# Optimization experiments

Hardware: AMD Instinct MI355X
Metric: run time of the kernel (lower is better)

The kernel has to match this reference:

```python
import jax, jax.numpy as jnp
import numpy as np

B, O, D = 4096, 256, 256  # batch, size_out (rules), size_in (features)


def setup_inputs() -> dict:
    key = jax.random.key(0)
    k1, k2, k3, k4, k5 = jax.random.split(key, 5)
    return {
        "x": jax.random.normal(k1, (B, D), dtype=jnp.float32),
        "scales": jax.random.normal(k2, (O, D), dtype=jnp.float32),
        # strict upper triangle holds the packed rot vectors (original inits them to zeros;
        # small values keep the quadratic form well conditioned)
        "rots": jax.random.normal(k3, (O, D, D), dtype=jnp.float32) * 0.02,
        "centroids": jax.random.normal(k4, (O, D, 1), dtype=jnp.float32),
        "b": jax.random.uniform(k5, (O,), dtype=jnp.float32, minval=0.5, maxval=1.5),
    }


def reference(x, scales, rots, centroids, b):
    # Build symmetric transform A[o] = diag(scales[o]) + triu(rots[o],1) + triu(rots[o],1)^T
    # (equivalent to the loop of diag_embed(r_i, i+1) + mirrored lower diagonal).
    upper = jnp.triu(rots, 1)                                   # [O,D,D]
    A = upper + jnp.swapaxes(upper, -1, -2)
    A = A + jnp.eye(D, dtype=scales.dtype) * scales[:, None, :]  # diag_embed(scales)
    # Augmented affine map: mul[o,i,b'] = A[o] @ x[b'] + centroid[o,i]; const row dropped
    # since only the first size_in rows feed the norm.
    y = jnp.einsum('bj,oij->boi', x, A) + centroids[..., 0][None, :, :]  # [B,O,D]
    rx = jnp.sqrt(jnp.sum(y * y, axis=-1))                      # L2 norm over D -> [B,O]
    return 1.0 / (1.0 + rx ** (2.0 * b))                        # bell membership [B,O]
```

## Files before the change

kernel.cpp:

```cpp
#include <hip/hip_runtime.h>
#include <cstdint>
#include <cmath>

#define Bn 4096
#define Dn 256
#define On 256

typedef __bf16 v8bf __attribute__((ext_vector_type(8)));
typedef float  v4f  __attribute__((ext_vector_type(4)));
typedef unsigned short us8 __attribute__((ext_vector_type(8)));

__device__ __forceinline__ unsigned short f2bf(float f) {
    unsigned int u = __builtin_bit_cast(unsigned int, f);
    unsigned int r = (u + 0x7fffu + ((u >> 16) & 1u)) >> 16;
    return (unsigned short)r;
}

__device__ __forceinline__ void gl_lds16(const void* g, void* l) {
    __builtin_amdgcn_global_load_lds(
        (const __attribute__((address_space(1))) void*)(uintptr_t)g,
        (__attribute__((address_space(3))) void*)(uintptr_t)l, 16, 0, 0);
}

__global__ __launch_bounds__(256) void prep(
    const float* __restrict__ scales, const float* __restrict__ rots,
    const float* __restrict__ x, unsigned short* __restrict__ Ap,
    unsigned short* __restrict__ xb) {
    const int bid = blockIdx.x;
    const int tid = threadIdx.x;

    if (bid >= 2560) {
        const int cb = bid - 2560;
#pragma unroll
        for (int s = 0; s < 4; ++s) {
            const int i = cb * 4096 + s * 1024 + tid * 4;
            const float4 v = *(const float4*)(x + i);
            ushort4 u;
            u.x = f2bf(v.x); u.y = f2bf(v.y); u.z = f2bf(v.z); u.w = f2bf(v.w);
            *(ushort4*)(xb + i) = u;
        }
        return;
    }

    static const int TI[10] = {0, 0, 0, 0, 1, 1, 1, 2, 2, 3};
    static const int TJ[10] = {0, 1, 2, 3, 1, 2, 3, 2, 3, 3};
    const int o  = bid / 10;
    const int p  = bid - o * 10;
    const int ti = TI[p], tj = TJ[p];

    __shared__ float t[64][68];
    const float* src = rots + (size_t)o * Dn * Dn + (size_t)(ti * 64) * Dn + tj * 64;
#pragma unroll
    for (int s = 0; s < 4; ++s) {
        const int idx = s * 256 + tid;
        const int r = idx >> 4, c = (idx & 15) * 4;
        const float4 v = *(const float4*)(src + r * Dn + c);
        *(float4*)&t[r][c] = v;
    }
    __syncthreads();

#pragma unroll
    for (int it = 0; it < 2; ++it) {
        const int slot = it * 256 + tid;
        const int bk = slot >> 6, L = slot & 63;
        const int quad = L >> 4, frow = L & 15;
        const int sl = bk >> 1, kl = bk & 1;
        const int r = sl * 16 + frow, c = kl * 32 + quad * 8;
        float v[8];
        if (ti == tj) {
#pragma unroll
            for (int q = 0; q < 8; ++q) {
                const int cc = c + q;
                v[q] = (r < cc) ? t[r][cc]
                     : ((r > cc) ? t[cc][r] : scales[o * Dn + ti * 64 + r]);
            }
        } else {
            const float4 a = *(const float4*)&t[r][c];
            const float4 b = *(const float4*)&t[r][c + 4];
            v[0] = a.x; v[1] = a.y; v[2] = a.z; v[3] = a.w;
            v[4] = b.x; v[5] = b.y; v[6] = b.z; v[7] = b.w;
        }
        us8 u;
#pragma unroll
        for (int q = 0; q < 8; ++q) u[q] = f2bf(v[q]);
        const size_t off = ((size_t)((o * 16 + ti * 4 + sl) * 8 + tj * 2 + kl)) * 512 + L * 8;
        *(us8*)(Ap + off) = u;
    }

    if (ti != tj) {
#pragma unroll
        for (int it = 0; it < 2; ++it) {
            const int slot = it * 256 + tid;
            const int bk = slot >> 6, L = slot & 63;
            const int quad = L >> 4, frow = L & 15;
            const int sl = bk >> 1, kl = bk & 1;
            const int r = sl * 16 + frow, c = kl * 32 + quad * 8;
            us8 u;
#pragma unroll
            for (int q = 0; q < 8; ++q) u[q] = f2bf(t[c + q][r]);
            const size_t off = ((size_t)((o * 16 + tj * 4 + sl) * 8 + ti * 2 + kl)) * 512 + L * 8;
            *(us8*)(Ap + off) = u;
        }
    }
}

__global__ __launch_bounds__(256, 2) void fuzzy_main(
    const unsigned short* __restrict__ Ap, const unsigned short* __restrict__ xb,
    const float* __restrict__ cent, const float* __restrict__ bvals,
    float* __restrict__ out) {
    __shared__ __align__(16) unsigned short Xs[2][4][64 * 64];
    __shared__ float ssbuf[2][4][64];
    __shared__ float centL[Dn];

    const int tid  = threadIdx.x;
    const int lane = tid & 63;
    const int wv   = tid >> 6;
    const int Lb = blockIdx.x;
    const int o     = (Lb & 7) * 32 + ((Lb >> 3) & 31);
    const int bhalf = Lb >> 8;

    centL[tid] = cent[o * Dn + tid];

    const int frow = lane & 15, quad = lane >> 4, f3 = lane & 7;
    const int lr = lane >> 3, ls = lane & 7;
    const int ksw = (ls ^ lr) * 8;

    const unsigned short* Aw = Ap + (size_t)(o * 16 + wv * 4) * 4096;
    v8bf af[4][8];
#pragma unroll
    for (int mi = 0; mi < 4; ++mi)
#pragma unroll
        for (int t = 0; t < 8; ++t)
            af[mi][t] = *(const v8bf*)(Aw + (size_t)(mi * 8 + t) * 512 + lane * 8);

    float cv[4][4];
#pragma unroll
    for (int mi = 0; mi < 4; ++mi)
#pragma unroll
        for (int rg = 0; rg < 4; ++rg)
            cv[mi][rg] = cent[o * Dn + wv * 64 + mi * 16 + quad * 4 + rg];

    {
        const int b0 = bhalf * 2048;
#pragma unroll
        for (int c = 0; c < 4; ++c)
#pragma unroll
            for (int q = 0; q < 2; ++q) {
                const int row = (wv * 2 + q) * 8 + lr;
                gl_lds16(xb + (size_t)(b0 + row) * Dn + c * 64 + ksw,
                         &Xs[0][c][row * 64 + ls * 8]);
            }
    }
    __syncthreads();

    for (int it = 0; it < 32; ++it) {
        const int buf = it & 1;
        const int b0  = bhalf * 2048 + it * 64;
        if (it < 31) {
            const int nb0 = b0 + 64;
#pragma unroll
            for (int c = 0; c < 4; ++c)
#pragma unroll
                for (int q = 0; q < 2; ++q) {
                    const int row = (wv * 2 + q) * 8 + lr;
                    gl_lds16(xb + (size_t)(nb0 + row) * Dn + c * 64 + ksw,
                             &Xs[buf ^ 1][c][row * 64 + ls * 8]);
                }
        }

        v4f acc[4][4];
#pragma unroll
        for (int mi = 0; mi < 4; ++mi)
#pragma unroll
            for (int ni = 0; ni < 4; ++ni)
                acc[mi][ni] = v4f{0.f, 0.f, 0.f, 0.f};

#pragma unroll
        for (int t = 0; t < 8; ++t) {
            v8bf xf[4];
            const int sl = ((t & 1) * 4 + quad) ^ f3;
#pragma unroll
            for (int ni = 0; ni < 4; ++ni)
                xf[ni] = *(const v8bf*)&Xs[buf][t >> 1][(ni * 16 + frow) * 64 + sl * 8];
#pragma unroll
            for (int mi = 0; mi < 4; ++mi)
#pragma unroll
                for (int ni = 0; ni < 4; ++ni)
                    acc[mi][ni] = __builtin_amdgcn_mfma_f32_16x16x32_bf16(
                        af[mi][t], xf[ni], acc[mi][ni], 0, 0, 0);
        }

#pragma unroll
        for (int ni = 0; ni < 4; ++ni) {
            float v = 0.f;
#pragma unroll
            for (int mi = 0; mi < 4; ++mi)
#pragma unroll
                for (int rg = 0; rg < 4; ++rg) {
                    const float y = acc[mi][ni][rg] + cv[mi][rg];
                    v += y * y;
                }
            v += __shfl_xor(v, 16);
            v += __shfl_xor(v, 32);
            if (lane < 16) ssbuf[buf][wv][ni * 16 + lane] = v;
        }
        __syncthreads();
        if (tid < 64) {
            const float ssq = ssbuf[buf][0][tid] + ssbuf[buf][1][tid] +
                              ssbuf[buf][2][tid] + ssbuf[buf][3][tid];
            out[(size_t)(b0 + tid) * On + o] = 1.0f / (1.0f + powf(ssq, bvals[o]));
        }
    }
}

__global__ void fallback_kernel(const float* __restrict__ x, const float* __restrict__ scales,
                                const float* __restrict__ rots, const float* __restrict__ cent,
                                const float* __restrict__ bvals, float* __restrict__ out) {
    const int b = blockIdx.x * blockDim.x + threadIdx.x;
    const int o = blockIdx.y;
    if (b >= Bn) return;
    const float* R  = rots + (size_t)o * Dn * Dn;
    const float* xv = x + (size_t)b * Dn;
    float ss = 0.f;
    for (int i = 0; i < Dn; ++i) {
        float a = cent[o * Dn + i];
        for (int j = 0; j < Dn; ++j) {
            const float w = (j > i) ? R[i * Dn + j]
                          : ((j < i) ? R[j * Dn + i] : scales[o * Dn + i]);
            a += w * xv[j];
        }
        ss += a * a;
    }
    out[(size_t)b * On + o] = 1.f / (1.f + powf(ss, bvals[o]));
}

extern "C" void kernel_launch(void* const* d_in, const int* in_sizes, int n_in,
                              void* d_out, int out_size, void* d_ws, size_t ws_size,
                              hipStream_t stream) {
    const float* x         = (const float*)d_in[0];
    const float* scales    = (const float*)d_in[1];
    const float* rots      = (const float*)d_in[2];
    const float* centroids = (const float*)d_in[3];
    const float* bvals     = (const float*)d_in[4];
    float* out = (float*)d_out;

    const size_t needA = (size_t)On * Dn * Dn * sizeof(unsigned short);
    const size_t needX = (size_t)Bn * Dn * sizeof(unsigned short);

    if (ws_size >= needA + needX) {
        unsigned short* Ap = (unsigned short*)d_ws;
        unsigned short* xb = (unsigned short*)((char*)d_ws + needA);
        prep<<<dim3(2816), 256, 0, stream>>>(scales, rots, x, Ap, xb);
        fuzzy_main<<<dim3(512), 256, 0, stream>>>(Ap, xb, centroids, bvals, out);
    } else {
        fallback_kernel<<<dim3(Bn / 256, On), 256, 0, stream>>>(x, scales, rots, centroids,
                                                                bvals, out);
    }
}
```

Measured before the change: 219.1 us.

## Fuse rots-to-bf16 A-fragment construction into main kernel via LDS staging

Removes the separate prep pass that wrote a packed bf16 copy of A to workspace. Each main block now streams the ten upper-triangular 64x64 fp32 tiles of rots into LDS with async global-to-LDS loads, triple buffered. Waves then build their register A-fragments directly, mirroring and transposing tiles as needed. This avoids the round trip of the 32MB bf16 A matrix through memory but makes each block read fp32 rots, and the two batch-half blocks for each o duplicate that read. It also adds ten barrier-separated stages before the GEMM loop.

```diff
diff --git a/kernel.cpp b/kernel.cpp
--- a/kernel.cpp
+++ b/kernel.cpp
@@ -22,95 +22,109 @@
         (__attribute__((address_space(3))) void*)(uintptr_t)l, 16, 0, 0);
 }
 
-__global__ __launch_bounds__(256) void prep(
-    const float* __restrict__ scales, const float* __restrict__ rots,
-    const float* __restrict__ x, unsigned short* __restrict__ Ap,
-    unsigned short* __restrict__ xb) {
-    const int bid = blockIdx.x;
+__global__ __launch_bounds__(256) void prep_x(const float* __restrict__ x,
+                                              unsigned short* __restrict__ xb) {
     const int tid = threadIdx.x;
-
-    if (bid >= 2560) {
-        const int cb = bid - 2560;
-#pragma unroll
-        for (int s = 0; s < 4; ++s) {
-            const int i = cb * 4096 + s * 1024 + tid * 4;
-            const float4 v = *(const float4*)(x + i);
-            ushort4 u;
-            u.x = f2bf(v.x); u.y = f2bf(v.y); u.z = f2bf(v.z); u.w = f2bf(v.w);
-            *(ushort4*)(xb + i) = u;
-        }
-        return;
-    }
-
-    static const int TI[10] = {0, 0, 0, 0, 1, 1, 1, 2, 2, 3};
-    static const int TJ[10] = {0, 1, 2, 3, 1, 2, 3, 2, 3, 3};
-    const int o  = bid / 10;
-    const int p  = bid - o * 10;
-    const int ti = TI[p], tj = TJ[p];
-
-    __shared__ float t[64][68];
-    const float* src = rots + (size_t)o * Dn * Dn + (size_t)(ti * 64) * Dn + tj * 64;
+    const int cb  = blockIdx.x;
 #pragma unroll
     for (int s = 0; s < 4; ++s) {
-        const int idx = s * 256 + tid;
-        const int r = idx >> 4, c = (idx & 15) * 4;
-        const float4 v = *(const float4*)(src + r * Dn + c);
-        *(float4*)&t[r][c] = v;
-    }
-    __syncthreads();
-
-#pragma unroll
-    for (int it = 0; it < 2; ++it) {
-        const int slot = it * 256 + tid;
-        const int bk = slot >> 6, L = slot & 63;
-        const int quad = L >> 4, frow = L & 15;
-        const int sl = bk >> 1, kl = bk & 1;
-        const int r = sl * 16 + frow, c = kl * 32 + quad * 8;
-        float v[8];
-        if (ti == tj) {
-#pragma unroll
-            for (int q = 0; q < 8; ++q) {
-                const int cc = c + q;
-                v[q] = (r < cc) ? t[r][cc]
-                     : ((r > cc) ? t[cc][r] : scales[o * Dn + ti * 64 + r]);
-            }
-        } else {
-            const float4 a = *(const float4*)&t[r][c];
-            const float4 b = *(const float4*)&t[r][c + 4];
-            v[0] = a.x; v[1] = a.y; v[2] = a.z; v[3] = a.w;
-            v[4] = b.x; v[5] = b.y; v[6] = b.z; v[7] = b.w;
-        }
-        us8 u;
-#pragma unroll
-        for (int q = 0; q < 8; ++q) u[q] = f2bf(v[q]);
-        const size_t off = ((size_t)((o * 16 + ti * 4 + sl) * 8 + tj * 2 + kl)) * 512 + L * 8;
-        *(us8*)(Ap + off) = u;
-    }
-
-    if (ti != tj) {
-#pragma unroll
-        for (int it = 0; it < 2; ++it) {
-            const int slot = it * 256 + tid;
-            const int bk = slot >> 6, L = slot & 63;
-            const int quad = L >> 4, frow = L & 15;
-            const int sl = bk >> 1, kl = bk & 1;
-            const int r = sl * 16 + frow, c = kl * 32 + quad * 8;
-            us8 u;
-#pragma unroll
-            for (int q = 0; q < 8; ++q) u[q] = f2bf(t[c + q][r]);
-            const size_t off = ((size_t)((o * 16 + tj * 4 + sl) * 8 + ti * 2 + kl)) * 512 + L * 8;
-            *(us8*)(Ap + off) = u;
-        }
-    }
-}
+        const int i = cb * 4096 + s * 1024 + tid * 4;
+        const float4 v = *(const float4*)(x + i);
+        ushort4 u;
+        u.x = f2bf(v.x); u.y = f2bf(v.y); u.z = f2bf(v.z); u.w = f2bf(v.w);
+        *(ushort4*)(xb + i) = u;
+    }
+}
+
+template <int TIv, int TJv>
+__device__ __forceinline__ void extract_pair(const float* T, v8bf (&af)[4][8],
+                                             const float (&sc4)[4],
+                                             int wv, int frow, int quad) {
+    if (TIv == TJv) {
+        if (wv == TIv) {
+#pragma unroll
+            for (int mi = 0; mi < 4; ++mi) {
+                const int r = mi * 16 + frow;
+#pragma unroll
+                for (int kl = 0; kl < 2; ++kl) {
+                    us8 u;
+#pragma unroll
+                    for (int q = 0; q < 8; ++q) {
+                        const int cc = kl * 32 + quad * 8 + q;
+                        const float v = (r < cc) ? T[r * 64 + cc]
+                                      : ((r > cc) ? T[cc * 64 + r] : sc4[mi]);
+                        u[q] = f2bf(v);
+                    }
+                    af[mi][TJv * 2 + kl] = __builtin_bit_cast(v8bf, u);
+                }
+            }
+        }
+    } else {
+        if (wv == TIv) {
+#pragma unroll
+            for (int mi = 0; mi < 4; ++mi) {
+                const int r = mi * 16 + frow;
+#pragma unroll
+                for (int kl = 0; kl < 2; ++kl) {
+                    const float4 a = *(const float4*)&T[r * 64 + kl * 32 + quad * 8];
+                    const float4 b = *(const float4*)&T[r * 64 + kl * 32 + quad * 8 + 4];
+                    us8 u;
+                    u[0] = f2bf(a.x); u[1] = f2bf(a.y); u[2] = f2bf(a.z); u[3] = f2bf(a.w);
+                    u[4] = f2bf(b.x); u[5] = f2bf(b.y); u[6] = f2bf(b.z); u[7] = f2bf(b.w);
+                    af[mi][TJv * 2 + kl] = __builtin_bit_cast(v8bf, u);
+                }
+            }
+        } else if (wv == TJv) {
+#pragma unroll
+            for (int mi = 0; mi < 4; ++mi) {
+                const int c = mi * 16 + frow;
+#pragma unroll
+                for (int kl = 0; kl < 2; ++kl) {
+                    us8 u;
+#pragma unroll
+                    for (int q = 0; q < 8; ++q)
+                        u[q] = f2bf(T[(kl * 32 + quad * 8 + q) * 64 + c]);
+                    af[mi][TIv * 2 + kl] = __builtin_bit_cast(v8bf, u);
+                }
+            }
+        }
+    }
+}
+
+#define WAITV(N)                                         \
+    do {                                                 \
+        asm volatile("s_waitcnt vmcnt(" #N ")" ::: "memory"); \
+        __builtin_amdgcn_sched_barrier(0);               \
+    } while (0)
+#define LGKM0()                                          \
+    do {                                                 \
+        asm volatile("s_waitcnt lgkmcnt(0)" ::: "memory"); \
+        __builtin_amdgcn_sched_barrier(0);               \
+    } while (0)
+#define BARF()                                           \
+    do {                                                 \
+        __builtin_amdgcn_sched_barrier(0);               \
+        __builtin_amdgcn_s_barrier();                    \
+        __builtin_amdgcn_sched_barrier(0);               \
+    } while (0)
+
+#define STAGE_T(TIv, TJv, SLOT)                                              \
+    do {                                                                     \
+        const float* s_ = rbase + (TIv) * (64 * Dn) + (TJv) * 64;            \
+        float* d_ = tileB + (SLOT) * 4096;                                   \
+        _Pragma("unroll")                                                    \
+        for (int s = 0; s < 4; ++s) {                                        \
+            const int idx = s * 256 + tid;                                   \
+            gl_lds16(s_ + (idx >> 4) * Dn + (idx & 15) * 4, d_ + idx * 4);   \
+        }                                                                    \
+    } while (0)
 
 __global__ __launch_bounds__(256, 2) void fuzzy_main(
-    const unsigned short* __restrict__ Ap, const unsigned short* __restrict__ xb,
-    const float* __restrict__ cent, const float* __restrict__ bvals,
-    float* __restrict__ out) {
+    const float* __restrict__ rots, const float* __restrict__ scales,
+    const unsigned short* __restrict__ xb, const float* __restrict__ cent,
+    const float* __restrict__ bvals, float* __restrict__ out) {
     __shared__ __align__(16) unsigned short Xs[2][4][64 * 64];
     __shared__ float ssbuf[2][4][64];
-    __shared__ float centL[Dn];
 
     const int tid  = threadIdx.x;
     const int lane = tid & 63;
@@ -119,26 +133,39 @@
     const int o     = (Lb & 7) * 32 + ((Lb >> 3) & 31);
     const int bhalf = Lb >> 8;
 
-    centL[tid] = cent[o * Dn + tid];
-
     const int frow = lane & 15, quad = lane >> 4, f3 = lane & 7;
     const int lr = lane >> 3, ls = lane & 7;
     const int ksw = (ls ^ lr) * 8;
 
-    const unsigned short* Aw = Ap + (size_t)(o * 16 + wv * 4) * 4096;
-    v8bf af[4][8];
-#pragma unroll
-    for (int mi = 0; mi < 4; ++mi)
-#pragma unroll
-        for (int t = 0; t < 8; ++t)
-            af[mi][t] = *(const v8bf*)(Aw + (size_t)(mi * 8 + t) * 512 + lane * 8);
-
     float cv[4][4];
 #pragma unroll
     for (int mi = 0; mi < 4; ++mi)
 #pragma unroll
         for (int rg = 0; rg < 4; ++rg)
             cv[mi][rg] = cent[o * Dn + wv * 64 + mi * 16 + quad * 4 + rg];
+
+    float sc4[4];
+#pragma unroll
+    for (int mi = 0; mi < 4; ++mi)
+        sc4[mi] = scales[o * Dn + wv * 64 + mi * 16 + frow];
+
+    float* const tileB = (float*)&Xs[0][0][0];
+    const float* const rbase = rots + ((size_t)o << 16);
+
+    v8bf af[4][8];
+
+    STAGE_T(0, 0, 0); STAGE_T(0, 1, 1); STAGE_T(0, 2, 2);
+
+    WAITV(8); BARF(); extract_pair<0, 0>(tileB + 0,    af, sc4, wv, frow, quad); LGKM0(); BARF(); STAGE_T(0, 3, 0);
+    WAITV(8); BARF(); extract_pair<0, 1>(tileB + 4096, af, sc4, wv, frow, quad); LGKM0(); BARF(); STAGE_T(1, 1, 1);
+    WAITV(8); BARF(); extract_pair<0, 2>(tileB + 8192, af, sc4, wv, frow, quad); LGKM0(); BARF(); STAGE_T(1, 2, 2);
+    WAITV(8); BARF(); extract_pair<0, 3>(tileB + 0,    af, sc4, wv, frow, quad); LGKM0(); BARF(); STAGE_T(1, 3, 0);
+    WAITV(8); BARF(); extract_pair<1, 1>(tileB + 4096, af, sc4, wv, frow, quad); LGKM0(); BARF(); STAGE_T(2, 2, 1);
+    WAITV(8); BARF(); extract_pair<1, 2>(tileB + 8192, af, sc4, wv, frow, quad); LGKM0(); BARF(); STAGE_T(2, 3, 2);
+    WAITV(8); BARF(); extract_pair<1, 3>(tileB + 0,    af, sc4, wv, frow, quad); LGKM0(); BARF(); STAGE_T(3, 3, 0);
+    WAITV(8); BARF(); extract_pair<2, 2>(tileB + 4096, af, sc4, wv, frow, quad); LGKM0(); BARF();
+    WAITV(4); BARF(); extract_pair<2, 3>(tileB + 8192, af, sc4, wv, frow, quad); LGKM0(); BARF();
+    WAITV(0); BARF(); extract_pair<3, 3>(tileB + 0,    af, sc4, wv, frow, quad); LGKM0(); BARF();
 
     {
         const int b0 = bhalf * 2048;
@@ -244,14 +271,12 @@
     const float* bvals     = (const float*)d_in[4];
     float* out = (float*)d_out;
 
-    const size_t needA = (size_t)On * Dn * Dn * sizeof(unsigned short);
     const size_t needX = (size_t)Bn * Dn * sizeof(unsigned short);
 
-    if (ws_size >= needA + needX) {
-        unsigned short* Ap = (unsigned short*)d_ws;
-        unsigned short* xb = (unsigned short*)((char*)d_ws + needA);
-        prep<<<dim3(2816), 256, 0, stream>>>(scales, rots, x, Ap, xb);
-        fuzzy_main<<<dim3(512), 256, 0, stream>>>(Ap, xb, centroids, bvals, out);
+    if (ws_size >= needX) {
+        unsigned short* xb = (unsigned short*)d_ws;
+        prep_x<<<dim3(256), 256, 0, stream>>>(x, xb);
+        fuzzy_main<<<dim3(512), 256, 0, stream>>>(rots, scales, xb, centroids, bvals, out);
     } else {
         fallback_kernel<<<dim3(Bn / 256, On), 256, 0, stream>>>(x, scales, rots, centroids,
                                                                 bvals, out);
```

Measured after the change: 227.3 us. 1.04x slower.
